# Kernel tuning notes

Hardware: AMD Instinct MI355X
Metric: run time of the kernel (lower is better)

## Reference

```python
import jax, jax.numpy as jnp
import numpy as np

N_NODES = 100000
N_EDGES = 3200000  # avg degree 32
D_IN = 128
D_OUT = 64


def setup_inputs() -> dict:
    key = jax.random.key(0)
    k1, k2, k3, k4, k5 = jax.random.split(key, 5)
    h = jax.random.normal(k1, (N_NODES, D_IN), dtype=jnp.float32)
    W = jax.random.normal(k2, (D_IN, D_OUT), dtype=jnp.float32) / np.float32(np.sqrt(D_IN))
    a = jax.random.normal(k3, (2 * D_OUT,), dtype=jnp.float32) / np.float32(np.sqrt(2 * D_OUT))
    src = jax.random.randint(k4, (N_EDGES,), 0, N_NODES, dtype=jnp.int32)
    dst = jax.random.randint(k5, (N_EDGES,), 0, N_NODES, dtype=jnp.int32)
    return {"h": h, "W": W, "a": a, "src": src, "dst": dst}


def reference(h, W, a, src, dst):
    N = h.shape[0]
    d = W.shape[1]
    # node projection: z = linear(h)  (bias-free, n_mlp_layer=1)
    z = h @ W  # [N, d]
    # edge attention logit: attn_linear(cat([z_src, z_dst])) == z_src@a[:d] + z_dst@a[d:]
    e = z[src] @ a[:d] + z[dst] @ a[d:]  # [E]
    # segment softmax over incoming edges of each destination node
    m = jax.ops.segment_max(e, dst, num_segments=N)  # [N]
    w = jnp.exp(e - m[dst])  # [E]
    s = jax.ops.segment_sum(w, dst, num_segments=N)  # [N]
    alpha = w / s[dst]  # [E]
    # weighted scatter-sum of source features (nodes with no in-edges stay 0, as in DGL)
    out = jax.ops.segment_sum(alpha[:, None] * z[src], dst, num_segments=N)  # [N, d]
    return out
```

## Files before the change

kernel.cpp:

```cpp
#include <hip/hip_runtime.h>

#define D_IN 128
#define D_OUT 64
#define SCAN_ITEMS 2048
#define TILE 4096
#define BSHIFT 7
#define NBK 128
#define MAXNB 1024
#define CAP 8192
#define BN 64
#define HS_STRIDE 132
#define MAXSB 1024

typedef float f32x4 __attribute__((ext_vector_type(4)));
typedef int   i32x4 __attribute__((ext_vector_type(4)));

__device__ __forceinline__ unsigned short f32_to_bf16(float f) {
    unsigned int u = __float_as_uint(f);
    u += 0x7fffu + ((u >> 16) & 1u);
    return (unsigned short)(u >> 16);
}

__global__ __launch_bounds__(256) void k_project(
    const float* __restrict__ h, const float* __restrict__ W,
    const float* __restrict__ a, unsigned short* __restrict__ z16,
    float* __restrict__ E, int n_nodes)
{
    __shared__ float ws[D_IN * D_OUT];
    __shared__ float hs[BN * HS_STRIDE];

    const int tid = threadIdx.x;
    const int nbase = blockIdx.x * BN;

#pragma unroll
    for (int i = 0; i < 8; ++i) {
        int f = (tid + 256 * i) * 4;
        *(float4*)&ws[f] = *(const float4*)&W[f];
    }
#pragma unroll
    for (int j = 0; j < 8; ++j) {
        int f = tid + 256 * j;
        int row = f >> 5;
        int kk = (f & 31) << 2;
        int gr = nbase + row;
        float4 v = make_float4(0.f, 0.f, 0.f, 0.f);
        if (gr < n_nodes) v = *(const float4*)&h[(size_t)gr * D_IN + kk];
        *(float4*)&hs[row * HS_STRIDE + kk] = v;
    }
    __syncthreads();

    const int c4 = (tid & 15) * 4;
    const int n4 = (tid >> 4) * 4;

    float acc[4][4];
#pragma unroll
    for (int i = 0; i < 4; ++i)
#pragma unroll
        for (int j = 0; j < 4; ++j) acc[i][j] = 0.0f;

    for (int k = 0; k < D_IN; k += 4) {
        float4 wv0 = *(float4*)&ws[(k + 0) * D_OUT + c4];
        float4 wv1 = *(float4*)&ws[(k + 1) * D_OUT + c4];
        float4 wv2 = *(float4*)&ws[(k + 2) * D_OUT + c4];
        float4 wv3 = *(float4*)&ws[(k + 3) * D_OUT + c4];
#pragma unroll
        for (int i = 0; i < 4; ++i) {
            float4 hv = *(float4*)&hs[(n4 + i) * HS_STRIDE + k];
            acc[i][0] = fmaf(hv.x, wv0.x, acc[i][0]);
            acc[i][1] = fmaf(hv.x, wv0.y, acc[i][1]);
            acc[i][2] = fmaf(hv.x, wv0.z, acc[i][2]);
            acc[i][3] = fmaf(hv.x, wv0.w, acc[i][3]);
            acc[i][0] = fmaf(hv.y, wv1.x, acc[i][0]);
            acc[i][1] = fmaf(hv.y, wv1.y, acc[i][1]);
            acc[i][2] = fmaf(hv.y, wv1.z, acc[i][2]);
            acc[i][3] = fmaf(hv.y, wv1.w, acc[i][3]);
            acc[i][0] = fmaf(hv.z, wv2.x, acc[i][0]);
            acc[i][1] = fmaf(hv.z, wv2.y, acc[i][1]);
            acc[i][2] = fmaf(hv.z, wv2.z, acc[i][2]);
            acc[i][3] = fmaf(hv.z, wv2.w, acc[i][3]);
            acc[i][0] = fmaf(hv.w, wv3.x, acc[i][0]);
            acc[i][1] = fmaf(hv.w, wv3.y, acc[i][1]);
            acc[i][2] = fmaf(hv.w, wv3.z, acc[i][2]);
            acc[i][3] = fmaf(hv.w, wv3.w, acc[i][3]);
        }
    }

    float a0 = a[c4 + 0], a1 = a[c4 + 1], a2 = a[c4 + 2], a3 = a[c4 + 3];
#pragma unroll
    for (int i = 0; i < 4; ++i) {
        int node = nbase + n4 + i;
        bool ok = node < n_nodes;
        if (ok) {
            ushort4 q;
            q.x = f32_to_bf16(acc[i][0]);
            q.y = f32_to_bf16(acc[i][1]);
            q.z = f32_to_bf16(acc[i][2]);
            q.w = f32_to_bf16(acc[i][3]);
            *(ushort4*)&z16[(size_t)node * D_OUT + c4] = q;
        }
        float es_p = acc[i][0] * a0 + acc[i][1] * a1 + acc[i][2] * a2 + acc[i][3] * a3;
        es_p += __shfl_xor(es_p, 1, 64);
        es_p += __shfl_xor(es_p, 2, 64);
        es_p += __shfl_xor(es_p, 4, 64);
        es_p += __shfl_xor(es_p, 8, 64);
        if ((tid & 15) == 0 && ok)
            E[node] = __expf(fminf(fmaxf(es_p, -60.0f), 60.0f));
    }
}

__global__ __launch_bounds__(512) void k_hist(
    const int* __restrict__ dst, unsigned int* __restrict__ histT,
    int n_edges, int NB, int NT)
{
    __shared__ unsigned int hcnt[MAXNB];
    int t = blockIdx.x;
    for (int b = threadIdx.x; b < NB; b += 512) hcnt[b] = 0;
    __syncthreads();
    int base = t * TILE;
    int lim = min(base + TILE, n_edges);
    for (int i = base + threadIdx.x * 4; i < lim; i += 2048) {
        if (i + 4 <= lim) {
            i32x4 d4 = __builtin_nontemporal_load((const i32x4*)&dst[i]);
            atomicAdd(&hcnt[(unsigned int)d4.x >> BSHIFT], 1u);
            atomicAdd(&hcnt[(unsigned int)d4.y >> BSHIFT], 1u);
            atomicAdd(&hcnt[(unsigned int)d4.z >> BSHIFT], 1u);
            atomicAdd(&hcnt[(unsigned int)d4.w >> BSHIFT], 1u);
        } else {
            for (int k = i; k < lim; ++k)
                atomicAdd(&hcnt[(unsigned int)dst[k] >> BSHIFT], 1u);
        }
    }
    __syncthreads();
    for (int b = threadIdx.x; b < NB; b += 512)
        histT[(size_t)b * NT + t] = hcnt[b];
}

__global__ __launch_bounds__(512) void k_partition(
    const int* __restrict__ src, const int* __restrict__ dst,
    const unsigned int* __restrict__ histT, unsigned int* __restrict__ tmp,
    int n_edges, int NB, int NT)
{
    __shared__ unsigned int cur[MAXNB];
    int t = blockIdx.x;
    for (int b = threadIdx.x; b < NB; b += 512)
        cur[b] = histT[(size_t)b * NT + t];
    __syncthreads();
    int base = t * TILE;
    int lim = min(base + TILE, n_edges);
    for (int i = base + threadIdx.x * 4; i < lim; i += 2048) {
        if (i + 4 <= lim) {
            i32x4 d4 = __builtin_nontemporal_load((const i32x4*)&dst[i]);
            i32x4 s4 = __builtin_nontemporal_load((const i32x4*)&src[i]);
            unsigned int d, pos;
            d = (unsigned int)d4.x;
            pos = atomicAdd(&cur[d >> BSHIFT], 1u);
            tmp[pos] = ((unsigned int)s4.x << BSHIFT) | (d & (NBK - 1u));
            d = (unsigned int)d4.y;
            pos = atomicAdd(&cur[d >> BSHIFT], 1u);
            tmp[pos] = ((unsigned int)s4.y << BSHIFT) | (d & (NBK - 1u));
            d = (unsigned int)d4.z;
            pos = atomicAdd(&cur[d >> BSHIFT], 1u);
            tmp[pos] = ((unsigned int)s4.z << BSHIFT) | (d & (NBK - 1u));
            d = (unsigned int)d4.w;
            pos = atomicAdd(&cur[d >> BSHIFT], 1u);
            tmp[pos] = ((unsigned int)s4.w << BSHIFT) | (d & (NBK - 1u));
        } else {
            for (int k = i; k < lim; ++k) {
                unsigned int d = (unsigned int)dst[k];
                unsigned int pos = atomicAdd(&cur[d >> BSHIFT], 1u);
                tmp[pos] = ((unsigned int)src[k] << BSHIFT) | (d & (NBK - 1u));
            }
        }
    }
}

__global__ __launch_bounds__(512) void k_gather(
    const unsigned int* __restrict__ tmp, const unsigned int* __restrict__ histT,
    const float* __restrict__ E, const unsigned short* __restrict__ z16,
    int* __restrict__ sscratch, float* __restrict__ out,
    int n_edges, int n_nodes, int NB, int NT)
{
    __shared__ unsigned int offL[NBK + 1];
    __shared__ unsigned int cnt[NBK];
    __shared__ unsigned int sedge[CAP];

    const int b = blockIdx.x;
    const int tid = threadIdx.x;
    const unsigned int s0 = histT[(size_t)b * NT];
    const unsigned int s1 = (b + 1 < NB) ? histT[(size_t)(b + 1) * NT] : (unsigned int)n_edges;
    const unsigned int sz = s1 - s0;
    const bool inLds = (sz <= CAP);

    unsigned int ev[16];
    if (inLds) {
#pragma unroll
        for (int j = 0; j < 16; ++j) {
            unsigned int i = s0 + (unsigned int)tid + 512u * (unsigned int)j;
            ev[j] = (i < s1) ? __builtin_nontemporal_load(&tmp[i]) : 0u;
        }
    }

    if (tid < NBK) cnt[tid] = 0;
    __syncthreads();
    if (inLds) {
#pragma unroll
        for (int j = 0; j < 16; ++j) {
            unsigned int i = s0 + (unsigned int)tid + 512u * (unsigned int)j;
            if (i < s1) atomicAdd(&cnt[ev[j] & (NBK - 1u)], 1u);
        }
    } else {
        for (unsigned int i = s0 + tid; i < s1; i += 512)
            atomicAdd(&cnt[tmp[i] & (NBK - 1u)], 1u);
    }
    __syncthreads();

    if (tid < 64) {
        unsigned int c0 = cnt[2 * tid], c1 = cnt[2 * tid + 1];
        unsigned int ps = c0 + c1;
        unsigned int run = ps;
#pragma unroll
        for (int o = 1; o < 64; o <<= 1) {
            unsigned int u = __shfl_up(run, o, 64);
            if (tid >= o) run += u;
        }
        unsigned int excl = run - ps;
        offL[2 * tid]     = excl;
        offL[2 * tid + 1] = excl + c0;
        cnt[2 * tid]      = excl;
        cnt[2 * tid + 1]  = excl + c0;
        if (tid == 63) offL[NBK] = run;
    }
    __syncthreads();

    if (inLds) {
#pragma unroll
        for (int j = 0; j < 16; ++j) {
            unsigned int i = s0 + (unsigned int)tid + 512u * (unsigned int)j;
            if (i < s1) {
                unsigned int val = ev[j];
                unsigned int pos = atomicAdd(&cnt[val & (NBK - 1u)], 1u);
                sedge[pos] = val >> BSHIFT;
            }
        }
    } else {
        for (unsigned int i = s0 + tid; i < s1; i += 512) {
            unsigned int val = tmp[i];
            unsigned int pos = atomicAdd(&cnt[val & (NBK - 1u)], 1u);
            sscratch[s0 + pos] = (int)(val >> BSHIFT);
        }
    }
    __syncthreads();

    const int wave = tid >> 6;
    const int lane = tid & 63;
    const int g = lane >> 3;
    const int fl = lane & 7;

    for (int dl = wave; dl < NBK; dl += 8) {
        int node = (b << BSHIFT) + dl;
        if (node >= n_nodes) break;
        unsigned int a0 = offL[dl], a1 = offL[dl + 1];
        float* orow = out + (size_t)node * D_OUT;
        if (a0 == a1) {
            if (g == 0) {
                __builtin_nontemporal_store((f32x4)0.f, (f32x4*)(orow + fl * 8));
                __builtin_nontemporal_store((f32x4)0.f, (f32x4*)(orow + fl * 8 + 4));
            }
            continue;
        }

        float acc[8];
#pragma unroll
        for (int j = 0; j < 8; ++j) acc[j] = 0.0f;
        float wsum = 0.0f;

        unsigned int i = a0 + (unsigned int)g;
        if (inLds) {
            for (; i + 8 < a1; i += 16) {
                int sn0 = (int)sedge[i];
                int sn1 = (int)sedge[i + 8];
                float w0 = E[sn0];
                float w1 = E[sn1];
                uint4 p0 = *(const uint4*)(z16 + (size_t)sn0 * D_OUT + fl * 8);
                uint4 p1 = *(const uint4*)(z16 + (size_t)sn1 * D_OUT + fl * 8);
                wsum += w0 + w1;
                const unsigned int pu0[4] = {p0.x, p0.y, p0.z, p0.w};
                const unsigned int pu1[4] = {p1.x, p1.y, p1.z, p1.w};
#pragma unroll
                for (int q = 0; q < 4; ++q) {
                    acc[2 * q]     = fmaf(w0, __uint_as_float(pu0[q] << 16),        acc[2 * q]);
                    acc[2 * q + 1] = fmaf(w0, __uint_as_float(pu0[q] & 0xffff0000u), acc[2 * q + 1]);
                    acc[2 * q]     = fmaf(w1, __uint_as_float(pu1[q] << 16),        acc[2 * q]);
                    acc[2 * q + 1] = fmaf(w1, __uint_as_float(pu1[q] & 0xffff0000u), acc[2 * q + 1]);
                }
            }
            if (i < a1) {
                int sn = (int)sedge[i];
                float w = E[sn];
                const uint4 p = *(const uint4*)(z16 + (size_t)sn * D_OUT + fl * 8);
                wsum += w;
                const unsigned int pu[4] = {p.x, p.y, p.z, p.w};
#pragma unroll
                for (int q = 0; q < 4; ++q) {
                    acc[2 * q]     = fmaf(w, __uint_as_float(pu[q] << 16),        acc[2 * q]);
                    acc[2 * q + 1] = fmaf(w, __uint_as_float(pu[q] & 0xffff0000u), acc[2 * q + 1]);
                }
            }
        } else {
            for (; i < a1; i += 8) {
                int sn = sscratch[s0 + i];
                float w = E[sn];
                const uint4 p = *(const uint4*)(z16 + (size_t)sn * D_OUT + fl * 8);
                wsum += w;
                const unsigned int pu[4] = {p.x, p.y, p.z, p.w};
#pragma unroll
                for (int q = 0; q < 4; ++q) {
                    acc[2 * q]     = fmaf(w, __uint_as_float(pu[q] << 16),        acc[2 * q]);
                    acc[2 * q + 1] = fmaf(w, __uint_as_float(pu[q] & 0xffff0000u), acc[2 * q + 1]);
                }
            }
        }

#pragma unroll
        for (int o = 8; o <= 32; o <<= 1) {
#pragma unroll
            for (int j = 0; j < 8; ++j) acc[j] += __shfl_xor(acc[j], o, 64);
            wsum += __shfl_xor(wsum, o, 64);
        }

        if (g == 0) {
            float inv = __builtin_amdgcn_rcpf(wsum);
            f32x4 o0 = {acc[0] * inv, acc[1] * inv, acc[2] * inv, acc[3] * inv};
            f32x4 o1 = {acc[4] * inv, acc[5] * inv, acc[6] * inv, acc[7] * inv};
            __builtin_nontemporal_store(o0, (f32x4*)(orow + fl * 8));
            __builtin_nontemporal_store(o1, (f32x4*)(orow + fl * 8 + 4));
        }
    }
}

__global__ __launch_bounds__(256) void k_rank(
    const int* __restrict__ dst, unsigned int* __restrict__ count,
    unsigned short* __restrict__ rank, int n_edges)
{
    int e = blockIdx.x * blockDim.x + threadIdx.x;
    if (e < n_edges) rank[e] = (unsigned short)atomicAdd(&count[dst[e]], 1u);
}

__global__ __launch_bounds__(256) void k_place(
    const int* __restrict__ src, const int* __restrict__ dst,
    const unsigned int* __restrict__ off, const unsigned short* __restrict__ rank,
    int* __restrict__ ssrc, int n_edges)
{
    int e = blockIdx.x * blockDim.x + threadIdx.x;
    if (e < n_edges) ssrc[off[dst[e]] + (unsigned int)rank[e]] = src[e];
}

__global__ __launch_bounds__(256) void k_count(
    const int* __restrict__ dst, unsigned int* __restrict__ count, int n_edges)
{
    int e = blockIdx.x * blockDim.x + threadIdx.x;
    if (e < n_edges) atomicAdd(&count[dst[e]], 1u);
}

__global__ __launch_bounds__(256) void k_fill(
    const int* __restrict__ src, const int* __restrict__ dst,
    unsigned int* __restrict__ cursor, int* __restrict__ ssrc, int n_edges)
{
    int e = blockIdx.x * blockDim.x + threadIdx.x;
    if (e < n_edges) {
        unsigned int pos = atomicAdd(&cursor[dst[e]], 1u);
        ssrc[pos] = src[e];
    }
}

__global__ __launch_bounds__(256) void k_fused(
    const int* __restrict__ ssrc, const unsigned int* __restrict__ off,
    const float* __restrict__ E, const unsigned short* __restrict__ z16,
    float* __restrict__ out, int n_nodes)
{
    int node = (blockIdx.x * blockDim.x + threadIdx.x) >> 6;
    int lane = threadIdx.x & 63;
    if (node >= n_nodes) return;
    int g  = lane >> 3;
    int fl = lane & 7;

    unsigned int start = off[node], end = off[node + 1];
    float* orow = out + (size_t)node * D_OUT;
    if (start == end) {
        if (g == 0) {
            *(float4*)(orow + fl * 8)     = make_float4(0.f, 0.f, 0.f, 0.f);
            *(float4*)(orow + fl * 8 + 4) = make_float4(0.f, 0.f, 0.f, 0.f);
        }
        return;
    }

    float acc[8];
#pragma unroll
    for (int j = 0; j < 8; ++j) acc[j] = 0.0f;
    float wsum = 0.0f;

    for (unsigned int i = start + g; i < end; i += 8) {
        int sn = ssrc[i];
        float w = E[sn];
        wsum += w;
        const uint4 p = *(const uint4*)(z16 + (size_t)sn * D_OUT + fl * 8);
        const unsigned int pu[4] = {p.x, p.y, p.z, p.w};
#pragma unroll
        for (int q = 0; q < 4; ++q) {
            float lo = __uint_as_float(pu[q] << 16);
            float hi = __uint_as_float(pu[q] & 0xffff0000u);
            acc[2 * q]     = fmaf(w, lo, acc[2 * q]);
            acc[2 * q + 1] = fmaf(w, hi, acc[2 * q + 1]);
        }
    }

#pragma unroll
    for (int o = 8; o <= 32; o <<= 1) {
#pragma unroll
        for (int j = 0; j < 8; ++j) acc[j] += __shfl_xor(acc[j], o, 64);
        wsum += __shfl_xor(wsum, o, 64);
    }

    if (g == 0) {
        float inv = 1.0f / wsum;
        float4 o0 = make_float4(acc[0] * inv, acc[1] * inv, acc[2] * inv, acc[3] * inv);
        float4 o1 = make_float4(acc[4] * inv, acc[5] * inv, acc[6] * inv, acc[7] * inv);
        *(float4*)(orow + fl * 8)     = o0;
        *(float4*)(orow + fl * 8 + 4) = o1;
    }
}

__global__ __launch_bounds__(256) void k_scan1(
    const unsigned int* __restrict__ count, unsigned int* __restrict__ off,
    unsigned int* __restrict__ blk_sums, int n)
{
    __shared__ unsigned int tmp[256];
    int tid = threadIdx.x;
    int base = blockIdx.x * SCAN_ITEMS;
    unsigned int v[8]; unsigned int tsum = 0;
#pragma unroll
    for (int i = 0; i < 8; ++i) {
        int idx = base + tid * 8 + i;
        v[i] = (idx < n) ? count[idx] : 0u;
        tsum += v[i];
    }
    tmp[tid] = tsum; __syncthreads();
    for (int o = 1; o < 256; o <<= 1) {
        unsigned int u = (tid >= o) ? tmp[tid - o] : 0u; __syncthreads();
        tmp[tid] += u; __syncthreads();
    }
    unsigned int run = tmp[tid] - tsum;
    if (tid == 255) blk_sums[blockIdx.x] = tmp[255];
#pragma unroll
    for (int i = 0; i < 8; ++i) {
        int idx = base + tid * 8 + i;
        if (idx < n) off[idx] = run;
        run += v[i];
    }
}

__global__ __launch_bounds__(256) void k_scan2(
    const unsigned int* __restrict__ blk_sums, unsigned int* __restrict__ blk_offs,
    unsigned int* __restrict__ off, int nblocks, int n)
{
    __shared__ unsigned int tmp[256];
    int tid = threadIdx.x;
    unsigned int carry = 0;
    for (int base = 0; base < nblocks; base += 256) {
        unsigned int v = (base + tid < nblocks) ? blk_sums[base + tid] : 0u;
        tmp[tid] = v; __syncthreads();
        for (int o = 1; o < 256; o <<= 1) {
            unsigned int u = (tid >= o) ? tmp[tid - o] : 0u; __syncthreads();
            tmp[tid] += u; __syncthreads();
        }
        if (base + tid < nblocks) blk_offs[base + tid] = carry + tmp[tid] - v;
        carry += tmp[255];
        __syncthreads();
    }
    if (tid == 0) off[n] = carry;
}

__global__ __launch_bounds__(256) void k_scan3(
    unsigned int* __restrict__ off, unsigned int* __restrict__ cursor,
    const unsigned int* __restrict__ blk_offs, int n)
{
    int i = blockIdx.x * blockDim.x + threadIdx.x;
    if (i < n) {
        unsigned int o = off[i] + blk_offs[i / SCAN_ITEMS];
        off[i] = o; cursor[i] = o;
    }
}

extern "C" void kernel_launch(void* const* d_in, const int* in_sizes, int n_in,
                              void* d_out, int out_size, void* d_ws, size_t ws_size,
                              hipStream_t stream) {
    const float* h   = (const float*)d_in[0];
    const float* W   = (const float*)d_in[1];
    const float* a   = (const float*)d_in[2];
    const int*   src = (const int*)d_in[3];
    const int*   dst = (const int*)d_in[4];
    float* out = (float*)d_out;

    const int n_nodes = in_sizes[0] / D_IN;
    const int n_edges = in_sizes[3];

    const int NB = (n_nodes + NBK - 1) >> BSHIFT;
    const int NT = (n_edges + TILE - 1) / TILE;
    const size_t histT_elems = (size_t)NB * NT + 1;
    const int n_scan = NB * NT;
    const int sb_sort = (n_scan + SCAN_ITEMS - 1) / SCAN_ITEMS;

    auto align = [](size_t x) { return (x + 255) & ~(size_t)255; };
    char* w = (char*)d_ws;
    unsigned short* z16 = (unsigned short*)w;  w += align((size_t)n_nodes * D_OUT * sizeof(unsigned short));
    float* E = (float*)w;                      w += align((size_t)n_nodes * sizeof(float));
    unsigned int* off = (unsigned int*)w;      w += align(((size_t)n_nodes + 1) * sizeof(unsigned int));
    unsigned int* blk_sums = (unsigned int*)w; w += align(MAXSB * sizeof(unsigned int));
    unsigned int* blk_offs = (unsigned int*)w; w += align(MAXSB * sizeof(unsigned int));
    size_t hist_region = align(((histT_elems > (size_t)n_nodes ? histT_elems : (size_t)n_nodes)) * sizeof(unsigned int));
    unsigned int* histT = (unsigned int*)w;    w += hist_region;
    unsigned int* count = histT;
    int* ssrc = (int*)w;                       w += align((size_t)n_edges * sizeof(int));
    unsigned int* tmp = (unsigned int*)w;
    unsigned short* rank = (unsigned short*)tmp;
    size_t need_sort = ((char*)tmp - (char*)d_ws) + align((size_t)n_edges * sizeof(unsigned int));
    size_t need_rank = ((char*)tmp - (char*)d_ws) + align((size_t)n_edges * sizeof(unsigned short));

    const bool use_sort = (ws_size >= need_sort) && NB <= MAXNB &&
                          n_nodes < (1 << 25) && sb_sort <= MAXSB;
    const bool use_rank = !use_sort && (ws_size >= need_rank);

    k_project<<<(n_nodes + BN - 1) / BN, 256, 0, stream>>>(h, W, a, z16, E, n_nodes);

    const int eblocks = (n_edges + 255) / 256;
    const int sb_node = (n_nodes + SCAN_ITEMS - 1) / SCAN_ITEMS;

    if (use_sort) {
        k_hist<<<NT, 512, 0, stream>>>(dst, histT, n_edges, NB, NT);
        k_scan1<<<sb_sort, 256, 0, stream>>>(histT, histT, blk_sums, n_scan);
        k_scan2<<<1, 256, 0, stream>>>(blk_sums, blk_offs, histT, sb_sort, n_scan);
        k_scan3<<<(n_scan + 255) / 256, 256, 0, stream>>>(histT, histT, blk_offs, n_scan);
        k_partition<<<NT, 512, 0, stream>>>(src, dst, histT, tmp, n_edges, NB, NT);
        k_gather<<<NB, 512, 0, stream>>>(tmp, histT, E, z16, ssrc, out,
                                         n_edges, n_nodes, NB, NT);
    } else if (use_rank) {
        hipMemsetAsync(count, 0, (size_t)n_nodes * sizeof(unsigned int), stream);
        k_rank<<<eblocks, 256, 0, stream>>>(dst, count, rank, n_edges);
        k_scan1<<<sb_node, 256, 0, stream>>>(count, off, blk_sums, n_nodes);
        k_scan2<<<1, 256, 0, stream>>>(blk_sums, blk_offs, off, sb_node, n_nodes);
        k_scan3<<<(n_nodes + 255) / 256, 256, 0, stream>>>(off, count, blk_offs, n_nodes);
        k_place<<<eblocks, 256, 0, stream>>>(src, dst, off, rank, ssrc, n_edges);
        k_fused<<<(n_nodes + 3) / 4, 256, 0, stream>>>(ssrc, off, E, z16, out, n_nodes);
    } else {
        hipMemsetAsync(count, 0, (size_t)n_nodes * sizeof(unsigned int), stream);
        k_count<<<eblocks, 256, 0, stream>>>(dst, count, n_edges);
        k_scan1<<<sb_node, 256, 0, stream>>>(count, off, blk_sums, n_nodes);
        k_scan2<<<1, 256, 0, stream>>>(blk_sums, blk_offs, off, sb_node, n_nodes);
        k_scan3<<<(n_nodes + 255) / 256, 256, 0, stream>>>(off, count, blk_offs, n_nodes);
        k_fill<<<eblocks, 256, 0, stream>>>(src, dst, count, ssrc, n_edges);
        k_fused<<<(n_nodes + 3) / 4, 256, 0, stream>>>(ssrc, off, E, z16, out, n_nodes);
    }
}
```

Baseline: 266.3 us.

## Replace per-tile histogram scan with global bucket totals and atomic offset reservation

The bucket-sort partition no longer stores a per-tile by per-bucket histogram and runs a three-kernel scan over it. Each tile's histogram is atomically added into global bucket totals, which a single small kernel scans. The partition kernel then recounts its tile in LDS and reserves per-bucket ranges with global atomics. The tile size is doubled to reduce block count, and the partition loads 16 edges per thread into registers. This removes several launches and a large scan, at the cost of nondeterministic edge order within buckets and global atomic contention.

```diff
diff --git a/kernel.cpp b/kernel.cpp
--- a/kernel.cpp
+++ b/kernel.cpp
@@ -3,7 +3,7 @@
 #define D_IN 128
 #define D_OUT 64
 #define SCAN_ITEMS 2048
-#define TILE 4096
+#define TILE 8192
 #define BSHIFT 7
 #define NBK 128
 #define MAXNB 1024
@@ -108,9 +108,9 @@
     }
 }
 
-__global__ __launch_bounds__(512) void k_hist(
-    const int* __restrict__ dst, unsigned int* __restrict__ histT,
-    int n_edges, int NB, int NT)
+__global__ __launch_bounds__(512) void k_hist2(
+    const int* __restrict__ dst, unsigned int* __restrict__ btot,
+    int n_edges, int NB)
 {
     __shared__ unsigned int hcnt[MAXNB];
     int t = blockIdx.x;
@@ -131,54 +131,104 @@
         }
     }
     __syncthreads();
-    for (int b = threadIdx.x; b < NB; b += 512)
-        histT[(size_t)b * NT + t] = hcnt[b];
-}
-
-__global__ __launch_bounds__(512) void k_partition(
+    for (int b = threadIdx.x; b < NB; b += 512) {
+        unsigned int c = hcnt[b];
+        if (c) atomicAdd(&btot[b], c);
+    }
+}
+
+__global__ __launch_bounds__(256) void k_bscan(
+    const unsigned int* __restrict__ btot, unsigned int* __restrict__ boff,
+    unsigned int* __restrict__ gcur, int nb)
+{
+    __shared__ unsigned int tmp[256];
+    int tid = threadIdx.x;
+    unsigned int v[8]; unsigned int tsum = 0;
+#pragma unroll
+    for (int j = 0; j < 8; ++j) {
+        int idx = tid * 8 + j;
+        v[j] = (idx < nb) ? btot[idx] : 0u;
+        tsum += v[j];
+    }
+    tmp[tid] = tsum; __syncthreads();
+    for (int o = 1; o < 256; o <<= 1) {
+        unsigned int u = (tid >= o) ? tmp[tid - o] : 0u; __syncthreads();
+        tmp[tid] += u; __syncthreads();
+    }
+    unsigned int run = tmp[tid] - tsum;
+#pragma unroll
+    for (int j = 0; j < 8; ++j) {
+        int idx = tid * 8 + j;
+        if (idx < nb) { boff[idx] = run; gcur[idx] = run; }
+        run += v[j];
+    }
+    if (tid == 255) boff[nb] = tmp[255];
+}
+
+__global__ __launch_bounds__(512) void k_partition2(
     const int* __restrict__ src, const int* __restrict__ dst,
-    const unsigned int* __restrict__ histT, unsigned int* __restrict__ tmp,
-    int n_edges, int NB, int NT)
-{
-    __shared__ unsigned int cur[MAXNB];
-    int t = blockIdx.x;
-    for (int b = threadIdx.x; b < NB; b += 512)
-        cur[b] = histT[(size_t)b * NT + t];
-    __syncthreads();
-    int base = t * TILE;
-    int lim = min(base + TILE, n_edges);
-    for (int i = base + threadIdx.x * 4; i < lim; i += 2048) {
+    unsigned int* __restrict__ gcur, unsigned int* __restrict__ tmp,
+    int n_edges, int NB)
+{
+    __shared__ unsigned int cnt[MAXNB];
+    const int t = blockIdx.x;
+    const int tid = threadIdx.x;
+    const int base = t * TILE;
+    const int lim = min(base + TILE, n_edges);
+
+    for (int b = tid; b < NB; b += 512) cnt[b] = 0;
+    __syncthreads();
+
+    unsigned int dv[16], sv[16];
+#pragma unroll
+    for (int j = 0; j < 4; ++j) {
+        int i = base + tid * 4 + j * 2048;
         if (i + 4 <= lim) {
             i32x4 d4 = __builtin_nontemporal_load((const i32x4*)&dst[i]);
             i32x4 s4 = __builtin_nontemporal_load((const i32x4*)&src[i]);
-            unsigned int d, pos;
-            d = (unsigned int)d4.x;
-            pos = atomicAdd(&cur[d >> BSHIFT], 1u);
-            tmp[pos] = ((unsigned int)s4.x << BSHIFT) | (d & (NBK - 1u));
-            d = (unsigned int)d4.y;
-            pos = atomicAdd(&cur[d >> BSHIFT], 1u);
-            tmp[pos] = ((unsigned int)s4.y << BSHIFT) | (d & (NBK - 1u));
-            d = (unsigned int)d4.z;
-            pos = atomicAdd(&cur[d >> BSHIFT], 1u);
-            tmp[pos] = ((unsigned int)s4.z << BSHIFT) | (d & (NBK - 1u));
-            d = (unsigned int)d4.w;
-            pos = atomicAdd(&cur[d >> BSHIFT], 1u);
-            tmp[pos] = ((unsigned int)s4.w << BSHIFT) | (d & (NBK - 1u));
+            dv[4 * j + 0] = (unsigned int)d4.x; sv[4 * j + 0] = (unsigned int)s4.x;
+            dv[4 * j + 1] = (unsigned int)d4.y; sv[4 * j + 1] = (unsigned int)s4.y;
+            dv[4 * j + 2] = (unsigned int)d4.z; sv[4 * j + 2] = (unsigned int)s4.z;
+            dv[4 * j + 3] = (unsigned int)d4.w; sv[4 * j + 3] = (unsigned int)s4.w;
         } else {
-            for (int k = i; k < lim; ++k) {
-                unsigned int d = (unsigned int)dst[k];
-                unsigned int pos = atomicAdd(&cur[d >> BSHIFT], 1u);
-                tmp[pos] = ((unsigned int)src[k] << BSHIFT) | (d & (NBK - 1u));
+#pragma unroll
+            for (int k = 0; k < 4; ++k) {
+                int ii = i + k;
+                bool ok = ii < lim;
+                dv[4 * j + k] = ok ? (unsigned int)dst[ii] : 0xFFFFFFFFu;
+                sv[4 * j + k] = ok ? (unsigned int)src[ii] : 0u;
             }
         }
     }
+
+#pragma unroll
+    for (int k = 0; k < 16; ++k) {
+        unsigned int d = dv[k];
+        if (d != 0xFFFFFFFFu) atomicAdd(&cnt[d >> BSHIFT], 1u);
+    }
+    __syncthreads();
+
+    for (int b = tid; b < NB; b += 512) {
+        unsigned int c = cnt[b];
+        cnt[b] = c ? atomicAdd(&gcur[b], c) : 0u;
+    }
+    __syncthreads();
+
+#pragma unroll
+    for (int k = 0; k < 16; ++k) {
+        unsigned int d = dv[k];
+        if (d != 0xFFFFFFFFu) {
+            unsigned int pos = atomicAdd(&cnt[d >> BSHIFT], 1u);
+            tmp[pos] = (sv[k] << BSHIFT) | (d & (NBK - 1u));
+        }
+    }
 }
 
 __global__ __launch_bounds__(512) void k_gather(
-    const unsigned int* __restrict__ tmp, const unsigned int* __restrict__ histT,
+    const unsigned int* __restrict__ tmp, const unsigned int* __restrict__ boff,
     const float* __restrict__ E, const unsigned short* __restrict__ z16,
     int* __restrict__ sscratch, float* __restrict__ out,
-    int n_edges, int n_nodes, int NB, int NT)
+    int n_edges, int n_nodes, int NB)
 {
     __shared__ unsigned int offL[NBK + 1];
     __shared__ unsigned int cnt[NBK];
@@ -186,8 +236,8 @@
 
     const int b = blockIdx.x;
     const int tid = threadIdx.x;
-    const unsigned int s0 = histT[(size_t)b * NT];
-    const unsigned int s1 = (b + 1 < NB) ? histT[(size_t)(b + 1) * NT] : (unsigned int)n_edges;
+    const unsigned int s0 = boff[b];
+    const unsigned int s1 = boff[b + 1];
     const unsigned int sz = s1 - s0;
     const bool inLds = (sz <= CAP);
 
@@ -288,9 +338,9 @@
                 const unsigned int pu1[4] = {p1.x, p1.y, p1.z, p1.w};
 #pragma unroll
                 for (int q = 0; q < 4; ++q) {
-                    acc[2 * q]     = fmaf(w0, __uint_as_float(pu0[q] << 16),        acc[2 * q]);
+                    acc[2 * q]     = fmaf(w0, __uint_as_float(pu0[q] << 16),         acc[2 * q]);
                     acc[2 * q + 1] = fmaf(w0, __uint_as_float(pu0[q] & 0xffff0000u), acc[2 * q + 1]);
-                    acc[2 * q]     = fmaf(w1, __uint_as_float(pu1[q] << 16),        acc[2 * q]);
+                    acc[2 * q]     = fmaf(w1, __uint_as_float(pu1[q] << 16),         acc[2 * q]);
                     acc[2 * q + 1] = fmaf(w1, __uint_as_float(pu1[q] & 0xffff0000u), acc[2 * q + 1]);
                 }
             }
@@ -302,7 +352,7 @@
                 const unsigned int pu[4] = {p.x, p.y, p.z, p.w};
 #pragma unroll
                 for (int q = 0; q < 4; ++q) {
-                    acc[2 * q]     = fmaf(w, __uint_as_float(pu[q] << 16),        acc[2 * q]);
+                    acc[2 * q]     = fmaf(w, __uint_as_float(pu[q] << 16),         acc[2 * q]);
                     acc[2 * q + 1] = fmaf(w, __uint_as_float(pu[q] & 0xffff0000u), acc[2 * q + 1]);
                 }
             }
@@ -315,7 +365,7 @@
                 const unsigned int pu[4] = {p.x, p.y, p.z, p.w};
 #pragma unroll
                 for (int q = 0; q < 4; ++q) {
-                    acc[2 * q]     = fmaf(w, __uint_as_float(pu[q] << 16),        acc[2 * q]);
+                    acc[2 * q]     = fmaf(w, __uint_as_float(pu[q] << 16),         acc[2 * q]);
                     acc[2 * q + 1] = fmaf(w, __uint_as_float(pu[q] & 0xffff0000u), acc[2 * q + 1]);
                 }
             }
@@ -506,9 +556,6 @@
 
     const int NB = (n_nodes + NBK - 1) >> BSHIFT;
     const int NT = (n_edges + TILE - 1) / TILE;
-    const size_t histT_elems = (size_t)NB * NT + 1;
-    const int n_scan = NB * NT;
-    const int sb_sort = (n_scan + SCAN_ITEMS - 1) / SCAN_ITEMS;
 
     auto align = [](size_t x) { return (x + 255) & ~(size_t)255; };
     char* w = (char*)d_ws;
@@ -517,8 +564,11 @@
     unsigned int* off = (unsigned int*)w;      w += align(((size_t)n_nodes + 1) * sizeof(unsigned int));
     unsigned int* blk_sums = (unsigned int*)w; w += align(MAXSB * sizeof(unsigned int));
     unsigned int* blk_offs = (unsigned int*)w; w += align(MAXSB * sizeof(unsigned int));
-    size_t hist_region = align(((histT_elems > (size_t)n_nodes ? histT_elems : (size_t)n_nodes)) * sizeof(unsigned int));
-    unsigned int* histT = (unsigned int*)w;    w += hist_region;
+    size_t hist_elems = (size_t)n_nodes > 8192 ? (size_t)n_nodes : (size_t)8192;
+    unsigned int* histT = (unsigned int*)w;    w += align(hist_elems * sizeof(unsigned int));
+    unsigned int* btot = histT;
+    unsigned int* boff = histT + 2048;
+    unsigned int* gcur = histT + 4352;
     unsigned int* count = histT;
     int* ssrc = (int*)w;                       w += align((size_t)n_edges * sizeof(int));
     unsigned int* tmp = (unsigned int*)w;
@@ -527,7 +577,7 @@
     size_t need_rank = ((char*)tmp - (char*)d_ws) + align((size_t)n_edges * sizeof(unsigned short));
 
     const bool use_sort = (ws_size >= need_sort) && NB <= MAXNB &&
-                          n_nodes < (1 << 25) && sb_sort <= MAXSB;
+                          n_nodes < (1 << 25);
     const bool use_rank = !use_sort && (ws_size >= need_rank);
 
     k_project<<<(n_nodes + BN - 1) / BN, 256, 0, stream>>>(h, W, a, z16, E, n_nodes);
@@ -536,13 +586,12 @@
     const int sb_node = (n_nodes + SCAN_ITEMS - 1) / SCAN_ITEMS;
 
     if (use_sort) {
-        k_hist<<<NT, 512, 0, stream>>>(dst, histT, n_edges, NB, NT);
-        k_scan1<<<sb_sort, 256, 0, stream>>>(histT, histT, blk_sums, n_scan);
-        k_scan2<<<1, 256, 0, stream>>>(blk_sums, blk_offs, histT, sb_sort, n_scan);
-        k_scan3<<<(n_scan + 255) / 256, 256, 0, stream>>>(histT, histT, blk_offs, n_scan);
-        k_partition<<<NT, 512, 0, stream>>>(src, dst, histT, tmp, n_edges, NB, NT);
-        k_gather<<<NB, 512, 0, stream>>>(tmp, histT, E, z16, ssrc, out,
-                                         n_edges, n_nodes, NB, NT);
+        hipMemsetAsync(btot, 0, (size_t)(NB + 1) * sizeof(unsigned int), stream);
+        k_hist2<<<NT, 512, 0, stream>>>(dst, btot, n_edges, NB);
+        k_bscan<<<1, 256, 0, stream>>>(btot, boff, gcur, NB);
+        k_partition2<<<NT, 512, 0, stream>>>(src, dst, gcur, tmp, n_edges, NB);
+        k_gather<<<NB, 512, 0, stream>>>(tmp, boff, E, z16, ssrc, out,
+                                         n_edges, n_nodes, NB);
     } else if (use_rank) {
         hipMemsetAsync(count, 0, (size_t)n_nodes * sizeof(unsigned int), stream);
         k_rank<<<eblocks, 256, 0, stream>>>(dst, count, rank, n_edges);
```

Result: faster. 246.7 us (-7.4%).
